# Performance work log

Measured on AMD Instinct MI355X. Metric: run time of the kernel, lower is better.

Reference implementation:

```python
import jax, jax.numpy as jnp
import numpy as np

# Faithful JAX translation of fastmax_function with mask=True, p=1, normalize=0.
# In that branch the torch code sets temperature = 1 and uses a0 = a1 = 1.

def setup_inputs() -> dict:
    key = jax.random.key(0)
    kq, kk, kv = jax.random.split(key, 3)
    b, h, n, d = 2, 8, 8192, 32
    q = jax.random.normal(kq, (b, h, n, d), dtype=jnp.float32)
    k = jax.random.normal(kk, (b, h, n, d), dtype=jnp.float32)
    v = jax.random.normal(kv, (b, h, n, d), dtype=jnp.float32)
    return {"q": q, "k": k, "v": v}


def reference(q, k, v):
    # q, k, v: (b, h, n, d); causal (mask=True), p=1, a0=a1=1, temperature=1
    b, h, n, d = q.shape
    # first term: running sum of values
    first = jnp.cumsum(v, axis=2)                                  # (b,h,n,d)
    # second term: q_i . (sum_{j<=i} k_j v_j^T)
    kv = jnp.einsum('bhnd,bhne->bhnde', k, v)                      # (b,h,n,d,d)
    kv_cs = jnp.cumsum(kv, axis=2)                                 # (b,h,n,d,d)
    second = jnp.einsum('bhnd,bhnde->bhne', q, kv_cs)              # (b,h,n,d)
    # denominator: i + q_i . (sum_{j<=i} k_j)
    k_cs = jnp.cumsum(k, axis=2)                                   # (b,h,n,d)
    div1 = jnp.arange(1, n + 1, dtype=q.dtype)                     # (n,)
    div2 = jnp.einsum('bhnd,bhnd->bhn', q, k_cs)                   # (b,h,n)
    div = (div1[None, None, :] + div2)[..., None]                  # (b,h,n,1)
    return (first + second) / div
```

## Files before the change

kernel.cpp:

```cpp
#include <hip/hip_runtime.h>


#define D      32
#define C      64
#define NCHUNK 128
#define BH     16
#define NBLK   (BH * NCHUNK)
#define STATE  1088

typedef __attribute__((ext_vector_type(8))) short bf16x8;
typedef __attribute__((ext_vector_type(4))) float f32x4;
typedef __attribute__((ext_vector_type(4))) unsigned short u16x4;

__device__ __forceinline__ unsigned short f2bf(float x) {
  union { float f; unsigned u; } c; c.f = x;
  unsigned r = (c.u + 0x7FFFu + ((c.u >> 16) & 1u)) >> 16;
  return (unsigned short)r;
}
__device__ __forceinline__ int permcol(int e) {
  return (e & 1) ? (16 + (e >> 1)) : (e >> 1);
}

__global__ __launch_bounds__(256) void chunk_kv_kernel(
    const float* __restrict__ k, const float* __restrict__ v,
    float* __restrict__ totals) {
  int blk = blockIdx.x;
  const float4* kp = (const float4*)k + (size_t)blk * 512;
  const float4* vp = (const float4*)v + (size_t)blk * 512;

  __shared__ __align__(16) unsigned short kT[D * 72];
  __shared__ __align__(16) unsigned short vT[D * 72];
  __shared__ __align__(16) float4 psK[256];
  __shared__ __align__(16) float4 psV[256];

  int t  = threadIdx.x;
  int j0 = t >> 3;
  int cb = (t & 7) * 4;
  int lane = t & 63, w = t >> 6;
  int m16 = lane & 15, quad = lane >> 4;
  int mb = w >> 1, nb = w & 1;
  int d1b = 16 * mb + quad * 4;
  int d2  = 16 * nb + m16;
  int n   = permcol(d2);

  float4 kA = kp[t], kB = kp[t + 256];
  float4 vA = vp[t], vB = vp[t + 256];

  {
    const float* ka = &kA.x; const float* kb = &kB.x;
    const float* va = &vA.x; const float* vb = &vB.x;
#pragma unroll
    for (int cc = 0; cc < 4; ++cc) {
      kT[(cb + cc) * 72 + j0]      = f2bf(ka[cc]);
      kT[(cb + cc) * 72 + j0 + 32] = f2bf(kb[cc]);
      vT[(cb + cc) * 72 + j0]      = f2bf(va[cc]);
      vT[(cb + cc) * 72 + j0 + 32] = f2bf(vb[cc]);
    }
    psK[t] = make_float4(kA.x + kB.x, kA.y + kB.y, kA.z + kB.z, kA.w + kB.w);
    psV[t] = make_float4(vA.x + vB.x, vA.y + vB.y, vA.z + vB.z, vA.w + vB.w);
  }
  __syncthreads();

  f32x4 acc = {0.f, 0.f, 0.f, 0.f};
#pragma unroll
  for (int kb2 = 0; kb2 < 2; ++kb2) {
    bf16x8 a = *(const bf16x8*)&kT[(16 * mb + m16) * 72 + kb2 * 32 + quad * 8];
    bf16x8 b = *(const bf16x8*)&vT[(16 * nb + m16) * 72 + kb2 * 32 + quad * 8];
    acc = __builtin_amdgcn_mfma_f32_16x16x32_bf16(a, b, acc, 0, 0, 0);
  }

  float* tp = totals + (size_t)blk * STATE;
  *(float4*)&tp[n * 32 + d1b] = make_float4(acc[0], acc[1], acc[2], acc[3]);
  if (t < 64) {
    int ee = t & 31;
    const float* ps = (t < 32) ? (const float*)psK : (const float*)psV;
    float csum = 0.f;
#pragma unroll
    for (int m = 0; m < 32; ++m) csum += ps[ee + 32 * m];
    tp[1024 + t] = csum;
  }
}

__global__ __launch_bounds__(256) void totals_scan_kernel(float* __restrict__ totals) {
  int gidx = blockIdx.x * 256 + threadIdx.x;
  int bh = gidx / STATE;
  int e  = gidx % STATE;
  float* base = totals + (size_t)(bh * NCHUNK) * STATE + e;
  float a = 0.f;
#pragma unroll 8
  for (int cc = 0; cc < NCHUNK; ++cc) {
    float s = base[(size_t)cc * STATE];
    base[(size_t)cc * STATE] = a;
    a += s;
  }
}

__global__ __launch_bounds__(256, 4) void output_kernel(
    const float* __restrict__ q, const float* __restrict__ k,
    const float* __restrict__ v, const float* __restrict__ totals,
    float* __restrict__ out) {
  int blk = blockIdx.x;
  int c   = blk & 127;
  size_t off = (size_t)blk * (C * D);
  const float4* qp4 = (const float4*)q + (size_t)blk * 512;
  const float4* kp4 = (const float4*)k + (size_t)blk * 512;
  const float4* vp4 = (const float4*)v + (size_t)blk * 512;
  const float* tbc = totals + (size_t)blk * STATE;

  __shared__ __align__(16) char uA[10240];
  unsigned short* qbf = (unsigned short*)uA;
  unsigned short* kbf = (unsigned short*)(uA + 5120);
  float* q_s = (float*)uA;
  __shared__ __align__(16) unsigned short vTbf[D * 72];
  __shared__ __align__(16) unsigned short kvTbf[D * 40];
  __shared__ __align__(16) unsigned short Tbf[C * 72];
  __shared__ __align__(16) float kc_s[C * 36];
  __shared__ __align__(16) float gtot[8 * 32];
  __shared__ __align__(16) float kpre_s[D], vpre_s[D], invdiv_s[C];

  int t  = threadIdx.x;
  int j0 = t >> 3;
  int cb = (t & 7) * 4;

  float4 qA = qp4[t], qB = qp4[t + 256];
  float4 kA = kp4[t], kB = kp4[t + 256];
  float4 vA = vp4[t], vB = vp4[t + 256];
  float4 tv4 = *(const float4*)&tbc[4 * t];
  float4 tail = make_float4(0.f, 0.f, 0.f, 0.f);
  if (t < 16) tail = *(const float4*)&tbc[1024 + 4 * t];

  for (int z = t; z < (C * 72) / 8; z += 256)
    ((uint4*)Tbf)[z] = make_uint4(0, 0, 0, 0);

  *(float4*)&kc_s[j0 * 36 + cb]        = kA;
  *(float4*)&kc_s[(j0 + 32) * 36 + cb] = kB;
  *(u16x4*)&qbf[j0 * 40 + cb] =
      (u16x4){f2bf(qA.x), f2bf(qA.y), f2bf(qA.z), f2bf(qA.w)};
  *(u16x4*)&qbf[(j0 + 32) * 40 + cb] =
      (u16x4){f2bf(qB.x), f2bf(qB.y), f2bf(qB.z), f2bf(qB.w)};
  *(u16x4*)&kbf[j0 * 40 + cb] =
      (u16x4){f2bf(kA.x), f2bf(kA.y), f2bf(kA.z), f2bf(kA.w)};
  *(u16x4*)&kbf[(j0 + 32) * 40 + cb] =
      (u16x4){f2bf(kB.x), f2bf(kB.y), f2bf(kB.z), f2bf(kB.w)};
  {
    const float* va = &vA.x; const float* vb = &vB.x;
#pragma unroll
    for (int cc = 0; cc < 4; ++cc) {
      int n = permcol(cb + cc);
      vTbf[n * 72 + j0]      = f2bf(va[cc]);
      vTbf[n * 72 + j0 + 32] = f2bf(vb[cc]);
    }
  }
  *(u16x4*)&kvTbf[(t >> 3) * 40 + (t & 7) * 4] =
      (u16x4){f2bf(tv4.x), f2bf(tv4.y), f2bf(tv4.z), f2bf(tv4.w)};
  if (t < 8)            ((float4*)kpre_s)[t]     = tail;
  else if (t < 16)      ((float4*)vpre_s)[t - 8] = tail;
  __syncthreads();

  int lane = t & 63, w = t >> 6;
  int m16 = lane & 15, quad = lane >> 4;

  const bf16x8 aQ = *(const bf16x8*)&qbf[(16 * w + m16) * 40 + quad * 8];
  for (int jb = 0; jb <= w; ++jb) {
    bf16x8 bK = *(const bf16x8*)&kbf[(16 * jb + m16) * 40 + quad * 8];
    f32x4 cS = {0.f, 0.f, 0.f, 0.f};
    cS = __builtin_amdgcn_mfma_f32_16x16x32_bf16(aQ, bK, cS, 0, 0, 0);
    int jcol = 16 * jb + m16;
#pragma unroll
    for (int reg = 0; reg < 4; ++reg) {
      int i = 16 * w + quad * 4 + reg;
      float tv = (jcol <= i) ? (1.f + cS[reg]) : 0.f;
      Tbf[i * 72 + jcol] = f2bf(tv);
    }
  }
  int rg = t >> 5;
  int e  = t & 31;
  float vals[8];
  {
    float run = 0.f;
#pragma unroll
    for (int r = 0; r < 8; ++r) {
      vals[r] = kc_s[(rg * 8 + r) * 36 + e];
      run += vals[r];
    }
    gtot[rg * 32 + e] = run;
  }
  __syncthreads();

  {
    float offv = kpre_s[e];
    for (int g2 = 0; g2 < rg; ++g2) offv += gtot[g2 * 32 + e];
    float cacc = offv;
#pragma unroll
    for (int r = 0; r < 8; ++r) {
      cacc += vals[r];
      kc_s[(rg * 8 + r) * 36 + e] = cacc;
    }
  }
  *(float4*)&q_s[j0 * 36 + cb]        = qA;
  *(float4*)&q_s[(j0 + 32) * 36 + cb] = qB;
  __syncthreads();

  if (t < 64) {
    int i = t;
    float dp = 0.f;
#pragma unroll
    for (int d4 = 0; d4 < 8; ++d4) {
      float4 qv = *(const float4*)&q_s[i * 36 + 4 * d4];
      float4 kc = *(const float4*)&kc_s[i * 36 + 4 * d4];
      dp += qv.x * kc.x + qv.y * kc.y + qv.z * kc.z + qv.w * kc.w;
    }
    invdiv_s[i] = 1.f / ((float)(c * C + i + 1) + dp);
  }
  f32x4 o0 = {0.f, 0.f, 0.f, 0.f}, o1 = {0.f, 0.f, 0.f, 0.f};
  {
    bf16x8 b0 = *(const bf16x8*)&kvTbf[(m16)      * 40 + quad * 8];
    bf16x8 b1 = *(const bf16x8*)&kvTbf[(16 + m16) * 40 + quad * 8];
    o0 = __builtin_amdgcn_mfma_f32_16x16x32_bf16(aQ, b0, o0, 0, 0, 0);
    o1 = __builtin_amdgcn_mfma_f32_16x16x32_bf16(aQ, b1, o1, 0, 0, 0);
  }
  int kbcnt = (w >= 2) ? 2 : 1;
  for (int kb2 = 0; kb2 < kbcnt; ++kb2) {
    bf16x8 aT = *(const bf16x8*)&Tbf[(16 * w + m16) * 72 + kb2 * 32 + quad * 8];
    bf16x8 b0 = *(const bf16x8*)&vTbf[(m16)      * 72 + kb2 * 32 + quad * 8];
    bf16x8 b1 = *(const bf16x8*)&vTbf[(16 + m16) * 72 + kb2 * 32 + quad * 8];
    o0 = __builtin_amdgcn_mfma_f32_16x16x32_bf16(aT, b0, o0, 0, 0, 0);
    o1 = __builtin_amdgcn_mfma_f32_16x16x32_bf16(aT, b1, o1, 0, 0, 0);
  }
  __syncthreads();

  int e0 = 2 * m16;
#pragma unroll
  for (int reg = 0; reg < 4; ++reg) {
    int i = 16 * w + quad * 4 + reg;
    float id = invdiv_s[i];
    float2 o;
    o.x = (vpre_s[e0]     + o0[reg]) * id;
    o.y = (vpre_s[e0 + 1] + o1[reg]) * id;
    *(float2*)&out[off + (size_t)i * D + e0] = o;
  }
}

extern "C" void kernel_launch(void* const* d_in, const int* in_sizes, int n_in,
                              void* d_out, int out_size, void* d_ws, size_t ws_size,
                              hipStream_t stream) {
  const float* q = (const float*)d_in[0];
  const float* k = (const float*)d_in[1];
  const float* v = (const float*)d_in[2];
  float* out = (float*)d_out;
  float* totals = (float*)d_ws;

  chunk_kv_kernel<<<NBLK, 256, 0, stream>>>(k, v, totals);
  totals_scan_kernel<<<(BH * STATE) / 256, 256, 0, stream>>>(totals);
  output_kernel<<<NBLK, 256, 0, stream>>>(q, k, v, totals, out);
}
```

Before: 109.6 us.

## Drop separate chunk-state scan kernel; sum prior chunk aggregates in output kernel

Removes the serial totals_scan kernel. Each output block now sums the per-chunk KV states (stored as bf16) of all earlier chunks itself. This cuts a kernel launch and the serial scan over 128 chunks, and halves the state storage. The cost is quadratic redundant reads, about 64 chunks on average per block. Summing in fp32 from bf16-rounded per-chunk states also changes precision slightly.

```diff
diff --git a/kernel.cpp b/kernel.cpp
--- a/kernel.cpp
+++ b/kernel.cpp
@@ -6,7 +6,7 @@
 #define NCHUNK 128
 #define BH     16
 #define NBLK   (BH * NCHUNK)
-#define STATE  1088
+#define AGGU   1152
 
 typedef __attribute__((ext_vector_type(8))) short bf16x8;
 typedef __attribute__((ext_vector_type(4))) float f32x4;
@@ -17,13 +17,17 @@
   unsigned r = (c.u + 0x7FFFu + ((c.u >> 16) & 1u)) >> 16;
   return (unsigned short)r;
 }
+__device__ __forceinline__ float bf2f(unsigned short u) {
+  union { unsigned u; float f; } c; c.u = ((unsigned)u) << 16;
+  return c.f;
+}
 __device__ __forceinline__ int permcol(int e) {
   return (e & 1) ? (16 + (e >> 1)) : (e >> 1);
 }
 
-__global__ __launch_bounds__(256) void chunk_kv_kernel(
+__global__ __launch_bounds__(256) void chunk_agg_kernel(
     const float* __restrict__ k, const float* __restrict__ v,
-    float* __restrict__ totals) {
+    unsigned short* __restrict__ agg) {
   int blk = blockIdx.x;
   const float4* kp = (const float4*)k + (size_t)blk * 512;
   const float4* vp = (const float4*)v + (size_t)blk * 512;
@@ -69,43 +73,31 @@
     acc = __builtin_amdgcn_mfma_f32_16x16x32_bf16(a, b, acc, 0, 0, 0);
   }
 
-  float* tp = totals + (size_t)blk * STATE;
-  *(float4*)&tp[n * 32 + d1b] = make_float4(acc[0], acc[1], acc[2], acc[3]);
+  unsigned short* ap = agg + (size_t)blk * AGGU;
+  *(u16x4*)&ap[n * 32 + d1b] =
+      (u16x4){f2bf(acc[0]), f2bf(acc[1]), f2bf(acc[2]), f2bf(acc[3])};
   if (t < 64) {
     int ee = t & 31;
     const float* ps = (t < 32) ? (const float*)psK : (const float*)psV;
     float csum = 0.f;
 #pragma unroll
     for (int m = 0; m < 32; ++m) csum += ps[ee + 32 * m];
-    tp[1024 + t] = csum;
-  }
-}
-
-__global__ __launch_bounds__(256) void totals_scan_kernel(float* __restrict__ totals) {
-  int gidx = blockIdx.x * 256 + threadIdx.x;
-  int bh = gidx / STATE;
-  int e  = gidx % STATE;
-  float* base = totals + (size_t)(bh * NCHUNK) * STATE + e;
-  float a = 0.f;
-#pragma unroll 8
-  for (int cc = 0; cc < NCHUNK; ++cc) {
-    float s = base[(size_t)cc * STATE];
-    base[(size_t)cc * STATE] = a;
-    a += s;
+    ((float*)(ap + 1024))[t] = csum;
   }
 }
 
 __global__ __launch_bounds__(256, 4) void output_kernel(
     const float* __restrict__ q, const float* __restrict__ k,
-    const float* __restrict__ v, const float* __restrict__ totals,
+    const float* __restrict__ v, const unsigned short* __restrict__ agg,
     float* __restrict__ out) {
   int blk = blockIdx.x;
   int c   = blk & 127;
+  int bh  = blk >> 7;
   size_t off = (size_t)blk * (C * D);
   const float4* qp4 = (const float4*)q + (size_t)blk * 512;
   const float4* kp4 = (const float4*)k + (size_t)blk * 512;
   const float4* vp4 = (const float4*)v + (size_t)blk * 512;
-  const float* tbc = totals + (size_t)blk * STATE;
+  const unsigned short* abh = agg + (size_t)(bh * NCHUNK) * AGGU;
 
   __shared__ __align__(16) char uA[10240];
   unsigned short* qbf = (unsigned short*)uA;
@@ -116,7 +108,8 @@
   __shared__ __align__(16) unsigned short Tbf[C * 72];
   __shared__ __align__(16) float kc_s[C * 36];
   __shared__ __align__(16) float gtot[8 * 32];
-  __shared__ __align__(16) float kpre_s[D], vpre_s[D], invdiv_s[C];
+  __shared__ __align__(16) float pre_s[64];
+  __shared__ __align__(16) float invdiv_s[C];
 
   int t  = threadIdx.x;
   int j0 = t >> 3;
@@ -125,9 +118,29 @@
   float4 qA = qp4[t], qB = qp4[t + 256];
   float4 kA = kp4[t], kB = kp4[t + 256];
   float4 vA = vp4[t], vB = vp4[t + 256];
-  float4 tv4 = *(const float4*)&tbc[4 * t];
-  float4 tail = make_float4(0.f, 0.f, 0.f, 0.f);
-  if (t < 16) tail = *(const float4*)&tbc[1024 + 4 * t];
+
+  float s0 = 0.f, s1 = 0.f, s2 = 0.f, s3 = 0.f;
+  float tf = 0.f;
+  for (int p0 = 0; p0 < c; p0 += 8) {
+    uint2 r[8]; float tl[8];
+#pragma unroll
+    for (int u = 0; u < 8; ++u) {
+      int p = p0 + u;
+      const unsigned short* apx = abh + (size_t)(p < c ? p : 0) * AGGU;
+      r[u] = *(const uint2*)&apx[4 * t];
+      if (t < 64) tl[u] = ((const float*)(apx + 1024))[t];
+    }
+#pragma unroll
+    for (int u = 0; u < 8; ++u) {
+      if (p0 + u < c) {
+        s0 += bf2f((unsigned short)(r[u].x & 0xffff));
+        s1 += bf2f((unsigned short)(r[u].x >> 16));
+        s2 += bf2f((unsigned short)(r[u].y & 0xffff));
+        s3 += bf2f((unsigned short)(r[u].y >> 16));
+        if (t < 64) tf += tl[u];
+      }
+    }
+  }
 
   for (int z = t; z < (C * 72) / 8; z += 256)
     ((uint4*)Tbf)[z] = make_uint4(0, 0, 0, 0);
@@ -152,9 +165,8 @@
     }
   }
   *(u16x4*)&kvTbf[(t >> 3) * 40 + (t & 7) * 4] =
-      (u16x4){f2bf(tv4.x), f2bf(tv4.y), f2bf(tv4.z), f2bf(tv4.w)};
-  if (t < 8)            ((float4*)kpre_s)[t]     = tail;
-  else if (t < 16)      ((float4*)vpre_s)[t - 8] = tail;
+      (u16x4){f2bf(s0), f2bf(s1), f2bf(s2), f2bf(s3)};
+  if (t < 64) pre_s[t] = tf;
   __syncthreads();
 
   int lane = t & 63, w = t >> 6;
@@ -188,7 +200,7 @@
   __syncthreads();
 
   {
-    float offv = kpre_s[e];
+    float offv = pre_s[e];
     for (int g2 = 0; g2 < rg; ++g2) offv += gtot[g2 * 32 + e];
     float cacc = offv;
 #pragma unroll
@@ -235,8 +247,8 @@
     int i = 16 * w + quad * 4 + reg;
     float id = invdiv_s[i];
     float2 o;
-    o.x = (vpre_s[e0]     + o0[reg]) * id;
-    o.y = (vpre_s[e0 + 1] + o1[reg]) * id;
+    o.x = (pre_s[32 + e0]     + o0[reg]) * id;
+    o.y = (pre_s[32 + e0 + 1] + o1[reg]) * id;
     *(float2*)&out[off + (size_t)i * D + e0] = o;
   }
 }
@@ -248,9 +260,8 @@
   const float* k = (const float*)d_in[1];
   const float* v = (const float*)d_in[2];
   float* out = (float*)d_out;
-  float* totals = (float*)d_ws;
-
-  chunk_kv_kernel<<<NBLK, 256, 0, stream>>>(k, v, totals);
-  totals_scan_kernel<<<(BH * STATE) / 256, 256, 0, stream>>>(totals);
-  output_kernel<<<NBLK, 256, 0, stream>>>(q, k, v, totals, out);
-}
+  unsigned short* agg = (unsigned short*)d_ws;
+
+  chunk_agg_kernel<<<NBLK, 256, 0, stream>>>(k, v, agg);
+  output_kernel<<<NBLK, 256, 0, stream>>>(q, k, v, agg, out);
+}
```

Result: slower. 122.0 us (+11.3%).
